# Kernel optimization log

Measured on AMD Instinct MI355X. Metric: run time of the kernel, lower is better.

Reference implementation:

```python
import jax, jax.numpy as jnp
import numpy as np

N = 50000          # num vertices
E = 20000          # num hyperedges
NNZ = 320000       # num incidences
IN_C = 256
HEADS = 8
OUT_C = 32
D = HEADS * OUT_C  # 256, projected feature dim


def setup_inputs() -> dict:
    key = jax.random.key(0)
    k1, k2, k3, k4 = jax.random.split(key, 4)
    X = jax.random.normal(k1, (N, IN_C), dtype=jnp.float32)
    vertex = jax.random.randint(k2, (NNZ,), 0, N, dtype=jnp.int64)
    edges = jax.random.randint(k3, (NNZ,), 0, E, dtype=jnp.int64)
    # Linear weight stored as [in, out] so projection is X @ W
    W = jax.random.normal(k4, (IN_C, D), dtype=jnp.float32) / np.sqrt(IN_C)
    eps = jnp.zeros((1,), dtype=jnp.float32)
    return {"X": X, "vertex": vertex, "edges": edges, "W": W, "eps": eps}


def reference(X, vertex, edges, W, eps):
    # Linear projection: [N, in] @ [in, heads*out] -> [N, D]
    Xp = X @ W
    # vertex -> edge: gather per-incidence vertex features, sum into hyperedges
    Xve = Xp[vertex]                                            # [NNZ, D]
    Xe = jax.ops.segment_sum(Xve, edges, num_segments=E)        # [E, D]
    # edge -> vertex: gather per-incidence edge features, sum into vertices
    Xev = Xe[edges]                                             # [NNZ, D]
    Xv = jax.ops.segment_sum(Xev, vertex, num_segments=N)       # [N, D]
    # GIN update
    return (1.0 + eps) * Xp + Xv
```

## Files before the change

kernel.cpp:

```cpp
#include <hip/hip_runtime.h>

constexpr int NV   = 50000;
constexpr int NE   = 20000;
constexpr int NNZI = 320000;
constexpr int KD   = 256;
constexpr int DD   = 256;
constexpr int ECAP = 64;
constexpr int VCAP = 32;

constexpr size_t alignup256(size_t x) { return (x + 255) & ~(size_t)255; }

constexpr size_t XPH_BYTES   = (size_t)NV * DD * 2;
constexpr size_t XEH_BYTES   = (size_t)NE * DD * 2;
constexpr size_t DEGV_BYTES  = alignup256((size_t)NV * sizeof(int));
constexpr size_t DEGE_BYTES  = alignup256((size_t)NE * sizeof(int));
constexpr size_t VLIST_BYTES = (size_t)NV * VCAP * sizeof(int);
constexpr size_t ELIST_BYTES = (size_t)NE * ECAP * sizeof(int);
constexpr size_t BPACK_ELEMS = 8ull * 16 * 64 * 8;
constexpr size_t BPACK_BYTES = BPACK_ELEMS * sizeof(unsigned short);

constexpr size_t XPH_OFF   = 0;
constexpr size_t XEH_OFF   = XPH_OFF + XPH_BYTES;
constexpr size_t DEGV_OFF  = XEH_OFF + XEH_BYTES;
constexpr size_t DEGE_OFF  = DEGV_OFF + DEGV_BYTES;
constexpr size_t VLIST_OFF = DEGE_OFF + DEGE_BYTES;
constexpr size_t ELIST_OFF = VLIST_OFF + VLIST_BYTES;
constexpr size_t BH_OFF    = ELIST_OFF + ELIST_BYTES;
constexpr size_t BL_OFF    = BH_OFF + BPACK_BYTES;

typedef float    floatx4 __attribute__((ext_vector_type(4)));
typedef short    shortx8 __attribute__((ext_vector_type(8)));
typedef _Float16 halfx4  __attribute__((ext_vector_type(4)));

static __device__ __forceinline__ unsigned short f2bf(float x) {
    unsigned int u = __float_as_uint(x);
    u = u + 0x7fffu + ((u >> 16) & 1u);
    return (unsigned short)(u >> 16);
}
static __device__ __forceinline__ float bf2f(unsigned short h) {
    return __uint_as_float(((unsigned int)h) << 16);
}

__global__ __launch_bounds__(256) void pack_w(
        const float* __restrict__ W,
        unsigned short* __restrict__ Bh, unsigned short* __restrict__ Bl) {
    const int idx  = blockIdx.x * 256 + threadIdx.x;
    const int k0   = idx >> 10;
    const int nt   = (idx >> 6) & 15;
    const int lane = idx & 63;
    const int krow = k0 * 32 + ((lane >> 4) << 3);
    const int ncol = nt * 16 + (lane & 15);
#pragma unroll
    for (int j = 0; j < 8; ++j) {
        const float w = W[(size_t)(krow + j) * DD + ncol];
        const unsigned short h = f2bf(w);
        Bh[(size_t)idx * 8 + j] = h;
        Bl[(size_t)idx * 8 + j] = f2bf(w - bf2f(h));
    }
}

__global__ __launch_bounds__(256) void gemm_mfma(
        const float* __restrict__ X,
        const unsigned short* __restrict__ Bh, const unsigned short* __restrict__ Bl,
        _Float16* __restrict__ Xp_h) {
    const int lane = threadIdx.x & 63;
    const int wv   = threadIdx.x >> 6;
    const int row_base = blockIdx.x * 64 + (wv >> 1) * 32;
    const int ntg0     = blockIdx.y * 8 + (wv & 1) * 4;

    floatx4 acc[2][4];
#pragma unroll
    for (int mt = 0; mt < 2; ++mt)
#pragma unroll
        for (int nt = 0; nt < 4; ++nt) acc[mt][nt] = (floatx4)0.f;

    const int lrow   = lane & 15;
    const int kgroup = (lane >> 4) << 3;

    int r0 = row_base + lrow;       if (r0 >= NV) r0 = NV - 1;
    int r1 = row_base + 16 + lrow;  if (r1 >= NV) r1 = NV - 1;
    const float* pA0 = &X[(size_t)r0 * KD + kgroup];
    const float* pA1 = &X[(size_t)r1 * KD + kgroup];

    for (int k0 = 0; k0 < 8; ++k0) {
        shortx8 bh[4], bl[4];
#pragma unroll
        for (int nt = 0; nt < 4; ++nt) {
            const size_t boff = ((size_t)(k0 * 16 + ntg0 + nt) * 64 + lane) * 8;
            bh[nt] = *reinterpret_cast<const shortx8*>(&Bh[boff]);
            bl[nt] = *reinterpret_cast<const shortx8*>(&Bl[boff]);
        }
        float xv[2][8];
        *reinterpret_cast<float4*>(&xv[0][0]) = *reinterpret_cast<const float4*>(pA0 + k0 * 32);
        *reinterpret_cast<float4*>(&xv[0][4]) = *reinterpret_cast<const float4*>(pA0 + k0 * 32 + 4);
        *reinterpret_cast<float4*>(&xv[1][0]) = *reinterpret_cast<const float4*>(pA1 + k0 * 32);
        *reinterpret_cast<float4*>(&xv[1][4]) = *reinterpret_cast<const float4*>(pA1 + k0 * 32 + 4);
        shortx8 ah[2], al[2];
#pragma unroll
        for (int mt = 0; mt < 2; ++mt)
#pragma unroll
            for (int j = 0; j < 8; ++j) {
                const unsigned short h = f2bf(xv[mt][j]);
                ah[mt][j] = (short)h;
                al[mt][j] = (short)f2bf(xv[mt][j] - bf2f(h));
            }
#pragma unroll
        for (int nt = 0; nt < 4; ++nt)
#pragma unroll
            for (int mt = 0; mt < 2; ++mt) {
                acc[mt][nt] = __builtin_amdgcn_mfma_f32_16x16x32_bf16(ah[mt], bh[nt], acc[mt][nt], 0, 0, 0);
                acc[mt][nt] = __builtin_amdgcn_mfma_f32_16x16x32_bf16(ah[mt], bl[nt], acc[mt][nt], 0, 0, 0);
                acc[mt][nt] = __builtin_amdgcn_mfma_f32_16x16x32_bf16(al[mt], bh[nt], acc[mt][nt], 0, 0, 0);
            }
    }

    const int rgroup = (lane >> 4) << 2;
#pragma unroll
    for (int mt = 0; mt < 2; ++mt) {
#pragma unroll
        for (int r = 0; r < 4; ++r) {
            const int row = row_base + mt * 16 + rgroup + r;
            if (row < NV) {
#pragma unroll
                for (int nt = 0; nt < 4; ++nt)
                    Xp_h[(size_t)row * DD + (ntg0 + nt) * 16 + (lane & 15)] =
                        (_Float16)acc[mt][nt][r];
            }
        }
    }
}

__global__ __launch_bounds__(256) void build_csr(
        const int* __restrict__ vertex, const int* __restrict__ edges,
        int* __restrict__ deg_v, int* __restrict__ deg_e,
        int* __restrict__ vlist, int* __restrict__ elist) {
    const int i = blockIdx.x * blockDim.x + threadIdx.x;
    if (i >= NNZI) return;
    const int v = vertex[i];
    const int e = edges[i];
    const int pe = atomicAdd(&deg_e[e], 1);
    if (pe < ECAP) elist[(size_t)e * ECAP + pe] = v;
    const int pv = atomicAdd(&deg_v[v], 1);
    if (pv < VCAP) vlist[(size_t)v * VCAP + pv] = e;
}

__global__ __launch_bounds__(256) void edge_gather(
        const _Float16* __restrict__ Xp_h, const int* __restrict__ deg_e,
        const int* __restrict__ elist, _Float16* __restrict__ Xe_h) {
    const int lane = threadIdx.x & 63;
    const int wid  = (blockIdx.x * blockDim.x + threadIdx.x) >> 6;
    if (wid >= NE) return;
    int cnt = deg_e[wid];
    if (cnt > ECAP) cnt = ECAP;
    const int idxl = elist[(size_t)wid * ECAP + lane];
    const int col  = lane * 4;
    float a0 = 0.f, a1 = 0.f, a2 = 0.f, a3 = 0.f;
    int j = 0;
    for (; j + 4 <= cnt; j += 4) {
        const int v0 = __shfl(idxl, j + 0);
        const int v1 = __shfl(idxl, j + 1);
        const int v2 = __shfl(idxl, j + 2);
        const int v3 = __shfl(idxl, j + 3);
        const halfx4 x0 = *reinterpret_cast<const halfx4*>(&Xp_h[(size_t)v0 * DD + col]);
        const halfx4 x1 = *reinterpret_cast<const halfx4*>(&Xp_h[(size_t)v1 * DD + col]);
        const halfx4 x2 = *reinterpret_cast<const halfx4*>(&Xp_h[(size_t)v2 * DD + col]);
        const halfx4 x3 = *reinterpret_cast<const halfx4*>(&Xp_h[(size_t)v3 * DD + col]);
        a0 += (float)x0[0] + (float)x1[0] + (float)x2[0] + (float)x3[0];
        a1 += (float)x0[1] + (float)x1[1] + (float)x2[1] + (float)x3[1];
        a2 += (float)x0[2] + (float)x1[2] + (float)x2[2] + (float)x3[2];
        a3 += (float)x0[3] + (float)x1[3] + (float)x2[3] + (float)x3[3];
    }
    for (; j < cnt; ++j) {
        const int v = __shfl(idxl, j);
        const halfx4 x = *reinterpret_cast<const halfx4*>(&Xp_h[(size_t)v * DD + col]);
        a0 += (float)x[0]; a1 += (float)x[1]; a2 += (float)x[2]; a3 += (float)x[3];
    }
    halfx4 o;
    o[0] = (_Float16)a0; o[1] = (_Float16)a1; o[2] = (_Float16)a2; o[3] = (_Float16)a3;
    *reinterpret_cast<halfx4*>(&Xe_h[(size_t)wid * DD + col]) = o;
}

__global__ __launch_bounds__(256) void vertex_gather(
        const _Float16* __restrict__ Xp_h, const _Float16* __restrict__ Xe_h,
        const int* __restrict__ deg_v, const int* __restrict__ vlist,
        const float* __restrict__ eps, float* __restrict__ out) {
    const int lane = threadIdx.x & 63;
    const int wid  = (blockIdx.x * blockDim.x + threadIdx.x) >> 6;
    if (wid >= NV) return;
    int cnt = deg_v[wid];
    if (cnt > VCAP) cnt = VCAP;
    const int idxl = vlist[(size_t)wid * VCAP + lane];
    const int col  = lane * 4;
    const float e1 = 1.0f + eps[0];
    const halfx4 xp = *reinterpret_cast<const halfx4*>(&Xp_h[(size_t)wid * DD + col]);
    float a0 = e1 * (float)xp[0], a1 = e1 * (float)xp[1];
    float a2 = e1 * (float)xp[2], a3 = e1 * (float)xp[3];
    int j = 0;
    for (; j + 4 <= cnt; j += 4) {
        const int e0 = __shfl(idxl, j + 0);
        const int e1i = __shfl(idxl, j + 1);
        const int e2 = __shfl(idxl, j + 2);
        const int e3 = __shfl(idxl, j + 3);
        const halfx4 t0 = *reinterpret_cast<const halfx4*>(&Xe_h[(size_t)e0 * DD + col]);
        const halfx4 t1 = *reinterpret_cast<const halfx4*>(&Xe_h[(size_t)e1i * DD + col]);
        const halfx4 t2 = *reinterpret_cast<const halfx4*>(&Xe_h[(size_t)e2 * DD + col]);
        const halfx4 t3 = *reinterpret_cast<const halfx4*>(&Xe_h[(size_t)e3 * DD + col]);
        a0 += (float)t0[0] + (float)t1[0] + (float)t2[0] + (float)t3[0];
        a1 += (float)t0[1] + (float)t1[1] + (float)t2[1] + (float)t3[1];
        a2 += (float)t0[2] + (float)t1[2] + (float)t2[2] + (float)t3[2];
        a3 += (float)t0[3] + (float)t1[3] + (float)t2[3] + (float)t3[3];
    }
    for (; j < cnt; ++j) {
        const int e = __shfl(idxl, j);
        const halfx4 t = *reinterpret_cast<const halfx4*>(&Xe_h[(size_t)e * DD + col]);
        a0 += (float)t[0]; a1 += (float)t[1]; a2 += (float)t[2]; a3 += (float)t[3];
    }
    float4 o; o.x = a0; o.y = a1; o.z = a2; o.w = a3;
    *reinterpret_cast<float4*>(&out[(size_t)wid * DD + col]) = o;
}

extern "C" void kernel_launch(void* const* d_in, const int* in_sizes, int n_in,
                              void* d_out, int out_size, void* d_ws, size_t ws_size,
                              hipStream_t stream) {
    const float* X      = (const float*)d_in[0];
    const int*   vertex = (const int*)d_in[1];
    const int*   edges  = (const int*)d_in[2];
    const float* W      = (const float*)d_in[3];
    const float* eps    = (const float*)d_in[4];
    float* out = (float*)d_out;
    char*  ws  = (char*)d_ws;

    _Float16* Xp_h = (_Float16*)(ws + XPH_OFF);
    _Float16* Xe_h = (_Float16*)(ws + XEH_OFF);
    int*   deg_v = (int*)(ws + DEGV_OFF);
    int*   deg_e = (int*)(ws + DEGE_OFF);
    int*   vlist = (int*)(ws + VLIST_OFF);
    int*   elist = (int*)(ws + ELIST_OFF);
    unsigned short* Bh = (unsigned short*)(ws + BH_OFF);
    unsigned short* Bl = (unsigned short*)(ws + BL_OFF);

    hipMemsetAsync(ws + DEGV_OFF, 0, DEGV_BYTES + DEGE_BYTES, stream);

    pack_w<<<32, 256, 0, stream>>>(W, Bh, Bl);
    gemm_mfma<<<dim3((NV + 63) / 64, 2), 256, 0, stream>>>(X, Bh, Bl, Xp_h);
    build_csr<<<(NNZI + 255) / 256, 256, 0, stream>>>(vertex, edges, deg_v, deg_e, vlist, elist);
    edge_gather<<<(NE + 3) / 4, 256, 0, stream>>>(Xp_h, deg_e, elist, Xe_h);
    vertex_gather<<<(NV + 3) / 4, 256, 0, stream>>>(Xp_h, Xe_h, deg_v, vlist, eps, out);
}
```

Before: 227.4 us.

## Use single-pass fp16 MFMA GEMM with prefetch and unroll gathers by eight

Replaces the three-pass split-bf16 GEMM (hi/lo emulation of fp32) with one fp16 MFMA per tile. W is packed once as fp16 and X is converted to fp16 in registers. Loads for the next k-step are double-buffered in registers. The edge and vertex gather loops are unrolled by eight with masked FMAs, so more independent gathers are in flight and there is no scalar tail. Dropping the hi/lo split lowers GEMM precision to plain fp16 inputs, which risks tolerance failures and overflow for large values. The masked tail also issues redundant loads of index 0.

```diff
diff --git a/kernel.cpp b/kernel.cpp
--- a/kernel.cpp
+++ b/kernel.cpp
@@ -17,7 +17,7 @@
 constexpr size_t VLIST_BYTES = (size_t)NV * VCAP * sizeof(int);
 constexpr size_t ELIST_BYTES = (size_t)NE * ECAP * sizeof(int);
 constexpr size_t BPACK_ELEMS = 8ull * 16 * 64 * 8;
-constexpr size_t BPACK_BYTES = BPACK_ELEMS * sizeof(unsigned short);
+constexpr size_t BPACK_BYTES = BPACK_ELEMS * 2;
 
 constexpr size_t XPH_OFF   = 0;
 constexpr size_t XEH_OFF   = XPH_OFF + XPH_BYTES;
@@ -25,25 +25,14 @@
 constexpr size_t DEGE_OFF  = DEGV_OFF + DEGV_BYTES;
 constexpr size_t VLIST_OFF = DEGE_OFF + DEGE_BYTES;
 constexpr size_t ELIST_OFF = VLIST_OFF + VLIST_BYTES;
-constexpr size_t BH_OFF    = ELIST_OFF + ELIST_BYTES;
-constexpr size_t BL_OFF    = BH_OFF + BPACK_BYTES;
+constexpr size_t BF_OFF    = ELIST_OFF + ELIST_BYTES;
 
 typedef float    floatx4 __attribute__((ext_vector_type(4)));
-typedef short    shortx8 __attribute__((ext_vector_type(8)));
+typedef _Float16 halfx8  __attribute__((ext_vector_type(8)));
 typedef _Float16 halfx4  __attribute__((ext_vector_type(4)));
 
-static __device__ __forceinline__ unsigned short f2bf(float x) {
-    unsigned int u = __float_as_uint(x);
-    u = u + 0x7fffu + ((u >> 16) & 1u);
-    return (unsigned short)(u >> 16);
-}
-static __device__ __forceinline__ float bf2f(unsigned short h) {
-    return __uint_as_float(((unsigned int)h) << 16);
-}
-
 __global__ __launch_bounds__(256) void pack_w(
-        const float* __restrict__ W,
-        unsigned short* __restrict__ Bh, unsigned short* __restrict__ Bl) {
+        const float* __restrict__ W, _Float16* __restrict__ Bf) {
     const int idx  = blockIdx.x * 256 + threadIdx.x;
     const int k0   = idx >> 10;
     const int nt   = (idx >> 6) & 15;
@@ -51,17 +40,12 @@
     const int krow = k0 * 32 + ((lane >> 4) << 3);
     const int ncol = nt * 16 + (lane & 15);
 #pragma unroll
-    for (int j = 0; j < 8; ++j) {
-        const float w = W[(size_t)(krow + j) * DD + ncol];
-        const unsigned short h = f2bf(w);
-        Bh[(size_t)idx * 8 + j] = h;
-        Bl[(size_t)idx * 8 + j] = f2bf(w - bf2f(h));
-    }
+    for (int j = 0; j < 8; ++j)
+        Bf[(size_t)idx * 8 + j] = (_Float16)W[(size_t)(krow + j) * DD + ncol];
 }
 
 __global__ __launch_bounds__(256) void gemm_mfma(
-        const float* __restrict__ X,
-        const unsigned short* __restrict__ Bh, const unsigned short* __restrict__ Bl,
+        const float* __restrict__ X, const _Float16* __restrict__ Bf,
         _Float16* __restrict__ Xp_h) {
     const int lane = threadIdx.x & 63;
     const int wv   = threadIdx.x >> 6;
@@ -82,36 +66,37 @@
     const float* pA0 = &X[(size_t)r0 * KD + kgroup];
     const float* pA1 = &X[(size_t)r1 * KD + kgroup];
 
-    for (int k0 = 0; k0 < 8; ++k0) {
-        shortx8 bh[4], bl[4];
+    float4 xb[2][2][2];
+    halfx8 bb[2][4];
+
+    auto loads = [&](int k0, int buf) {
+        xb[buf][0][0] = *reinterpret_cast<const float4*>(pA0 + k0 * 32);
+        xb[buf][0][1] = *reinterpret_cast<const float4*>(pA0 + k0 * 32 + 4);
+        xb[buf][1][0] = *reinterpret_cast<const float4*>(pA1 + k0 * 32);
+        xb[buf][1][1] = *reinterpret_cast<const float4*>(pA1 + k0 * 32 + 4);
 #pragma unroll
         for (int nt = 0; nt < 4; ++nt) {
             const size_t boff = ((size_t)(k0 * 16 + ntg0 + nt) * 64 + lane) * 8;
-            bh[nt] = *reinterpret_cast<const shortx8*>(&Bh[boff]);
-            bl[nt] = *reinterpret_cast<const shortx8*>(&Bl[boff]);
-        }
-        float xv[2][8];
-        *reinterpret_cast<float4*>(&xv[0][0]) = *reinterpret_cast<const float4*>(pA0 + k0 * 32);
-        *reinterpret_cast<float4*>(&xv[0][4]) = *reinterpret_cast<const float4*>(pA0 + k0 * 32 + 4);
-        *reinterpret_cast<float4*>(&xv[1][0]) = *reinterpret_cast<const float4*>(pA1 + k0 * 32);
-        *reinterpret_cast<float4*>(&xv[1][4]) = *reinterpret_cast<const float4*>(pA1 + k0 * 32 + 4);
-        shortx8 ah[2], al[2];
-#pragma unroll
-        for (int mt = 0; mt < 2; ++mt)
-#pragma unroll
-            for (int j = 0; j < 8; ++j) {
-                const unsigned short h = f2bf(xv[mt][j]);
-                ah[mt][j] = (short)h;
-                al[mt][j] = (short)f2bf(xv[mt][j] - bf2f(h));
-            }
+            bb[buf][nt] = *reinterpret_cast<const halfx8*>(&Bf[boff]);
+        }
+    };
+
+    loads(0, 0);
+    for (int k0 = 0; k0 < 8; ++k0) {
+        const int cur = k0 & 1;
+        if (k0 < 7) loads(k0 + 1, cur ^ 1);
+        halfx8 a[2];
+#pragma unroll
+        for (int mt = 0; mt < 2; ++mt) {
+            const float* xp = reinterpret_cast<const float*>(&xb[cur][mt][0]);
+#pragma unroll
+            for (int j = 0; j < 8; ++j) a[mt][j] = (_Float16)xp[j];
+        }
 #pragma unroll
         for (int nt = 0; nt < 4; ++nt)
 #pragma unroll
-            for (int mt = 0; mt < 2; ++mt) {
-                acc[mt][nt] = __builtin_amdgcn_mfma_f32_16x16x32_bf16(ah[mt], bh[nt], acc[mt][nt], 0, 0, 0);
-                acc[mt][nt] = __builtin_amdgcn_mfma_f32_16x16x32_bf16(ah[mt], bl[nt], acc[mt][nt], 0, 0, 0);
-                acc[mt][nt] = __builtin_amdgcn_mfma_f32_16x16x32_bf16(al[mt], bh[nt], acc[mt][nt], 0, 0, 0);
-            }
+            for (int mt = 0; mt < 2; ++mt)
+                acc[mt][nt] = __builtin_amdgcn_mfma_f32_16x16x32_f16(a[mt], bb[cur][nt], acc[mt][nt], 0, 0, 0);
     }
 
     const int rgroup = (lane >> 4) << 2;
@@ -155,25 +140,19 @@
     const int idxl = elist[(size_t)wid * ECAP + lane];
     const int col  = lane * 4;
     float a0 = 0.f, a1 = 0.f, a2 = 0.f, a3 = 0.f;
-    int j = 0;
-    for (; j + 4 <= cnt; j += 4) {
-        const int v0 = __shfl(idxl, j + 0);
-        const int v1 = __shfl(idxl, j + 1);
-        const int v2 = __shfl(idxl, j + 2);
-        const int v3 = __shfl(idxl, j + 3);
-        const halfx4 x0 = *reinterpret_cast<const halfx4*>(&Xp_h[(size_t)v0 * DD + col]);
-        const halfx4 x1 = *reinterpret_cast<const halfx4*>(&Xp_h[(size_t)v1 * DD + col]);
-        const halfx4 x2 = *reinterpret_cast<const halfx4*>(&Xp_h[(size_t)v2 * DD + col]);
-        const halfx4 x3 = *reinterpret_cast<const halfx4*>(&Xp_h[(size_t)v3 * DD + col]);
-        a0 += (float)x0[0] + (float)x1[0] + (float)x2[0] + (float)x3[0];
-        a1 += (float)x0[1] + (float)x1[1] + (float)x2[1] + (float)x3[1];
-        a2 += (float)x0[2] + (float)x1[2] + (float)x2[2] + (float)x3[2];
-        a3 += (float)x0[3] + (float)x1[3] + (float)x2[3] + (float)x3[3];
-    }
-    for (; j < cnt; ++j) {
-        const int v = __shfl(idxl, j);
-        const halfx4 x = *reinterpret_cast<const halfx4*>(&Xp_h[(size_t)v * DD + col]);
-        a0 += (float)x[0]; a1 += (float)x[1]; a2 += (float)x[2]; a3 += (float)x[3];
+    for (int base = 0; base < cnt; base += 8) {
+#pragma unroll
+        for (int jj = 0; jj < 8; ++jj) {
+            const int j   = base + jj;
+            const int sel = j < cnt ? j : 0;
+            const float s = j < cnt ? 1.f : 0.f;
+            const int v = __shfl(idxl, sel);
+            const halfx4 x = *reinterpret_cast<const halfx4*>(&Xp_h[(size_t)v * DD + col]);
+            a0 = fmaf(s, (float)x[0], a0);
+            a1 = fmaf(s, (float)x[1], a1);
+            a2 = fmaf(s, (float)x[2], a2);
+            a3 = fmaf(s, (float)x[3], a3);
+        }
     }
     halfx4 o;
     o[0] = (_Float16)a0; o[1] = (_Float16)a1; o[2] = (_Float16)a2; o[3] = (_Float16)a3;
@@ -195,25 +174,19 @@
     const halfx4 xp = *reinterpret_cast<const halfx4*>(&Xp_h[(size_t)wid * DD + col]);
     float a0 = e1 * (float)xp[0], a1 = e1 * (float)xp[1];
     float a2 = e1 * (float)xp[2], a3 = e1 * (float)xp[3];
-    int j = 0;
-    for (; j + 4 <= cnt; j += 4) {
-        const int e0 = __shfl(idxl, j + 0);
-        const int e1i = __shfl(idxl, j + 1);
-        const int e2 = __shfl(idxl, j + 2);
-        const int e3 = __shfl(idxl, j + 3);
-        const halfx4 t0 = *reinterpret_cast<const halfx4*>(&Xe_h[(size_t)e0 * DD + col]);
-        const halfx4 t1 = *reinterpret_cast<const halfx4*>(&Xe_h[(size_t)e1i * DD + col]);
-        const halfx4 t2 = *reinterpret_cast<const halfx4*>(&Xe_h[(size_t)e2 * DD + col]);
-        const halfx4 t3 = *reinterpret_cast<const halfx4*>(&Xe_h[(size_t)e3 * DD + col]);
-        a0 += (float)t0[0] + (float)t1[0] + (float)t2[0] + (float)t3[0];
-        a1 += (float)t0[1] + (float)t1[1] + (float)t2[1] + (float)t3[1];
-        a2 += (float)t0[2] + (float)t1[2] + (float)t2[2] + (float)t3[2];
-        a3 += (float)t0[3] + (float)t1[3] + (float)t2[3] + (float)t3[3];
-    }
-    for (; j < cnt; ++j) {
-        const int e = __shfl(idxl, j);
-        const halfx4 t = *reinterpret_cast<const halfx4*>(&Xe_h[(size_t)e * DD + col]);
-        a0 += (float)t[0]; a1 += (float)t[1]; a2 += (float)t[2]; a3 += (float)t[3];
+    for (int base = 0; base < cnt; base += 8) {
+#pragma unroll
+        for (int jj = 0; jj < 8; ++jj) {
+            const int j   = base + jj;
+            const int sel = j < cnt ? j : 0;
+            const float s = j < cnt ? 1.f : 0.f;
+            const int e = __shfl(idxl, sel);
+            const halfx4 t = *reinterpret_cast<const halfx4*>(&Xe_h[(size_t)e * DD + col]);
+            a0 = fmaf(s, (float)t[0], a0);
+            a1 = fmaf(s, (float)t[1], a1);
+            a2 = fmaf(s, (float)t[2], a2);
+            a3 = fmaf(s, (float)t[3], a3);
+        }
     }
     float4 o; o.x = a0; o.y = a1; o.z = a2; o.w = a3;
     *reinterpret_cast<float4*>(&out[(size_t)wid * DD + col]) = o;
@@ -236,13 +209,12 @@
     int*   deg_e = (int*)(ws + DEGE_OFF);
     int*   vlist = (int*)(ws + VLIST_OFF);
     int*   elist = (int*)(ws + ELIST_OFF);
-    unsigned short* Bh = (unsigned short*)(ws + BH_OFF);
-    unsigned short* Bl = (unsigned short*)(ws + BL_OFF);
+    _Float16* Bf  = (_Float16*)(ws + BF_OFF);
 
     hipMemsetAsync(ws + DEGV_OFF, 0, DEGV_BYTES + DEGE_BYTES, stream);
 
-    pack_w<<<32, 256, 0, stream>>>(W, Bh, Bl);
-    gemm_mfma<<<dim3((NV + 63) / 64, 2), 256, 0, stream>>>(X, Bh, Bl, Xp_h);
+    pack_w<<<32, 256, 0, stream>>>(W, Bf);
+    gemm_mfma<<<dim3((NV + 63) / 64, 2), 256, 0, stream>>>(X, Bf, Xp_h);
     build_csr<<<(NNZI + 255) / 256, 256, 0, stream>>>(vertex, edges, deg_v, deg_e, vlist, elist);
     edge_gather<<<(NE + 3) / 4, 256, 0, stream>>>(Xp_h, deg_e, elist, Xe_h);
     vertex_gather<<<(NV + 3) / 4, 256, 0, stream>>>(Xp_h, Xe_h, deg_v, vlist, eps, out);
```

Measured after the change: 217.3 us. -4.4%, faster.
